# Kernel tuning notes

Hardware: AMD Instinct MI355X
Metric: run time of the kernel (lower is better)

The kernel has to match this reference:

```python
import jax, jax.numpy as jnp
import numpy as np

N = 50000      # nodes
E = 400000     # edges (before self-loops)
IN = 128       # in_channels
H = 4          # heads
C = 64         # hidden_channels == out_channels (per head)
ELI = 200000   # link-prediction query edges
NEG_SLOPE = 0.2
EPS = 1e-5


def setup_inputs():
    key = jax.random.key(0)
    ks = jax.random.split(key, 20)
    sc = 0.05
    inp = {}
    inp["x"] = jax.random.normal(ks[0], (N, IN), jnp.float32)
    inp["edge_index"] = jax.random.randint(ks[1], (2, E), 0, N)
    inp["edge_label_index"] = jax.random.randint(ks[2], (2, ELI), 0, N)
    # layer 1 GATv2 params
    inp["Wl1"] = jax.random.normal(ks[3], (IN, H * C), jnp.float32) * sc
    inp["bl1"] = jnp.zeros((H * C,), jnp.float32)
    inp["Wr1"] = jax.random.normal(ks[4], (IN, H * C), jnp.float32) * sc
    inp["br1"] = jnp.zeros((H * C,), jnp.float32)
    inp["att1"] = jax.random.normal(ks[5], (H, C), jnp.float32) * sc
    inp["bias1"] = jnp.zeros((C,), jnp.float32)
    # norm1 (BatchNorm affine)
    inp["g1"] = jnp.ones((C,), jnp.float32)
    inp["b1"] = jnp.zeros((C,), jnp.float32)
    # residual projection 1 (in_channels 128 -> hidden_dim 64)
    inp["Wres"] = jax.random.normal(ks[6], (IN, C), jnp.float32) * sc
    inp["bres"] = jnp.zeros((C,), jnp.float32)
    # layer 2 GATv2 params (hidden_dim 64 -> out 64)
    inp["Wl2"] = jax.random.normal(ks[7], (C, H * C), jnp.float32) * sc
    inp["bl2"] = jnp.zeros((H * C,), jnp.float32)
    inp["Wr2"] = jax.random.normal(ks[8], (C, H * C), jnp.float32) * sc
    inp["br2"] = jnp.zeros((H * C,), jnp.float32)
    inp["att2"] = jax.random.normal(ks[9], (H, C), jnp.float32) * sc
    inp["bias2"] = jnp.zeros((C,), jnp.float32)
    # norm2
    inp["g2"] = jnp.ones((C,), jnp.float32)
    inp["b2"] = jnp.zeros((C,), jnp.float32)
    return inp


def _gatv2(x, src, dst, Wl, bl, Wr, br, att, bias, n):
    # PyG GATv2Conv, concat=False (mean over heads), dropout off (eval)
    xl = (x @ Wl + bl).reshape(n, H, -1)   # source transform
    xr = (x @ Wr + br).reshape(n, H, -1)   # target transform
    e = jax.nn.leaky_relu(xl[src] + xr[dst], NEG_SLOPE)      # [E,H,C]
    logits = jnp.einsum('ehc,hc->eh', e, att)                # [E,H]
    m = jax.ops.segment_max(logits, dst, num_segments=n)     # segment softmax
    p = jnp.exp(logits - m[dst])
    s = jax.ops.segment_sum(p, dst, num_segments=n)
    alpha = p / s[dst]                                       # [E,H]
    out = jax.ops.segment_sum(xl[src] * alpha[:, :, None], dst, num_segments=n)
    return out.mean(axis=1) + bias                           # [N,C]


def _bn(x, g, b):
    mu = x.mean(axis=0)
    var = x.var(axis=0)
    return g * (x - mu) * jax.lax.rsqrt(var + EPS) + b


def reference(x, edge_index, edge_label_index,
              Wl1, bl1, Wr1, br1, att1, bias1, g1, b1, Wres, bres,
              Wl2, bl2, Wr2, br2, att2, bias2, g2, b2):
    loop = jnp.arange(N)
    src = jnp.concatenate([edge_index[0], loop])  # add_self_loops=True
    dst = jnp.concatenate([edge_index[1], loop])
    x_res = x @ Wres + bres
    h = _gatv2(x, src, dst, Wl1, bl1, Wr1, br1, att1, bias1, N)
    h = jax.nn.relu(_bn(h, g1, b1) + x_res)
    # res_proj2 is Identity (hidden_dim == out_dim)
    h2 = _gatv2(h, src, dst, Wl2, bl2, Wr2, br2, att2, bias2, N)
    z = _bn(h2, g2, b2) + h
    scores = (z[edge_label_index[0]] * z[edge_label_index[1]]).sum(axis=-1)
    return jax.nn.sigmoid(scores)
```

## Files before the change

### kernel.cpp

```cpp
#include <hip/hip_runtime.h>
#include <math.h>

#define NN 50000
#define EE 400000
#define ETOT 450000
#define INC 128
#define CC 64
#define HC 256
#define ELI_N 200000
#define MPAD 50176

typedef unsigned short u16;
typedef __attribute__((ext_vector_type(8))) short short8v;
typedef __attribute__((ext_vector_type(8))) unsigned short u16x8;
typedef __attribute__((ext_vector_type(4))) float f32x4;
typedef __attribute__((ext_vector_type(4))) unsigned short u16x4;

__device__ __forceinline__ u16 f2b(float v){
    unsigned u = __float_as_uint(v);
    u = (u + 0x7fffu + ((u >> 16) & 1u)) >> 16;
    return (u16)u;
}
__device__ __forceinline__ float b2f(u16 h){
    return __uint_as_float(((unsigned)h) << 16);
}
__device__ __forceinline__ u16 f2h(float v){
    _Float16 h = (_Float16)v; u16 r; __builtin_memcpy(&r, &h, 2); return r;
}
__device__ __forceinline__ float h2f(u16 h){
    _Float16 x; __builtin_memcpy(&x, &h, 2); return (float)x;
}
__device__ __forceinline__ f32x4 h2f4(u16x4 r){
    f32x4 o; o[0]=h2f(r[0]); o[1]=h2f(r[1]); o[2]=h2f(r[2]); o[3]=h2f(r[3]); return o;
}

__global__ void k_setup(const float* __restrict__ x, const int* __restrict__ ei,
                        const float* __restrict__ Wl1, const float* __restrict__ Wr1,
                        const float* __restrict__ Wres, const float* __restrict__ Wl2,
                        const float* __restrict__ Wr2,
                        u16* __restrict__ xhi, u16* __restrict__ xlo,
                        u16* __restrict__ hl1, u16* __restrict__ ll1,
                        u16* __restrict__ hr1, u16* __restrict__ lr1,
                        u16* __restrict__ hres, u16* __restrict__ lres,
                        u16* __restrict__ hl2, u16* __restrict__ ll2,
                        u16* __restrict__ hr2, u16* __restrict__ lr2,
                        int* __restrict__ deg){
    int gid = blockIdx.x*256 + threadIdx.x;
    if (gid < 800000){
        int row = gid >> 4;
        int k0  = (gid & 15) * 8;
        const float* ap = x + (size_t)row*128 + k0;
        float4 v0 = *(const float4*)ap;
        float4 v1 = *(const float4*)(ap + 4);
        float vv[8] = {v0.x, v0.y, v0.z, v0.w, v1.x, v1.y, v1.z, v1.w};
        u16x8 h8, l8;
        #pragma unroll
        for (int j = 0; j < 8; j++){
            u16 h = f2b(vv[j]);
            h8[j] = h;
            l8[j] = f2b(vv[j] - b2f(h));
        }
        size_t blk = (size_t)(row >> 4)*4 + (k0 >> 5);
        size_t addr = blk*512 + (size_t)((row & 15) + 16*((k0 >> 3) & 3))*8;
        *(u16x8*)(xhi + addr) = h8;
        *(u16x8*)(xlo + addr) = l8;
    } else if (gid < 906496){
        int g = gid - 800000;
        const float* src; u16* dh; u16* dl; int K, N, idx;
        if      (g <  32768){ src=Wl1;  dh=hl1;  dl=ll1;  K=128; N=256; idx=g; }
        else if (g <  65536){ src=Wr1;  dh=hr1;  dl=lr1;  K=128; N=256; idx=g-32768; }
        else if (g <  73728){ src=Wres; dh=hres; dl=lres; K=128; N=64;  idx=g-65536; }
        else if (g <  90112){ src=Wl2;  dh=hl2;  dl=ll2;  K=64;  N=256; idx=g-73728; }
        else                { src=Wr2;  dh=hr2;  dl=lr2;  K=64;  N=256; idx=g-90112; }
        int k = idx / N, n = idx - k*N;
        float v = src[idx];
        u16 h = f2b(v);
        size_t blk = (size_t)(n >> 4)*(K >> 5) + (k >> 5);
        size_t addr = blk*512 + (size_t)((n & 15) + 16*((k >> 3) & 3))*8 + (k & 7);
        dh[addr] = h;
        dl[addr] = f2b(v - b2f(h));
    } else if (gid < 1306496){
        int e = gid - 906496;
        atomicAdd(&deg[ei[EE + e]], 1);
    }
}

__global__ void k_scanA(const int* __restrict__ deg, int* __restrict__ iscan, int* __restrict__ part){
    __shared__ int sh[256];
    int tid = threadIdx.x;
    int base = blockIdx.x*1024 + tid*4;
    int v[4]; int t = 0;
    #pragma unroll
    for (int i = 0; i < 4; i++){ int idx = base + i; v[i] = (idx < NN) ? deg[idx]+1 : 0; t += v[i]; }
    sh[tid] = t; __syncthreads();
    for (int off = 1; off < 256; off <<= 1){
        int u = (tid >= off) ? sh[tid - off] : 0;
        __syncthreads();
        sh[tid] += u;
        __syncthreads();
    }
    int incl = sh[tid];
    int run = incl - t;
    #pragma unroll
    for (int i = 0; i < 4; i++){
        run += v[i];
        int idx = base + i;
        if (idx < NN) iscan[idx] = run;
    }
    if (tid == 255) part[blockIdx.x] = incl;
}

__global__ void k_scanC(const int* __restrict__ iscan, const int* __restrict__ part,
                        const int* __restrict__ deg, int* __restrict__ rowptr, int* __restrict__ cursor){
    int chunk = blockIdx.x >> 2;
    int ps = 0;
    for (int j = 0; j < chunk; j++) ps += part[j];
    int i = blockIdx.x*256 + threadIdx.x;
    if (i < NN){
        int v = iscan[i] + ps;
        rowptr[i+1] = v;
        cursor[i] = v - (deg[i]+1);
    }
    if (i == 0) rowptr[0] = 0;
}

__global__ void k_fill(const int* __restrict__ ei, int* __restrict__ cursor, int* __restrict__ csr_src){
    int idx = blockIdx.x*256 + threadIdx.x;
    if (idx >= ETOT) return;
    int s, d;
    if (idx < EE){ s = ei[idx]; d = ei[EE + idx]; }
    else         { s = idx - EE; d = s; }
    int pos = atomicAdd(&cursor[d], 1);
    csr_src[pos] = s;
}

#define LSTR 80

__global__ __launch_bounds__(256) void k_gemm1(const u16* __restrict__ Ahi, const u16* __restrict__ Alo,
        const u16* __restrict__ Whl1, const u16* __restrict__ Wll1,
        const u16* __restrict__ Whr1, const u16* __restrict__ Wlr1,
        const u16* __restrict__ Whres,const u16* __restrict__ Wlres,
        const float* __restrict__ bl1, const float* __restrict__ br1, const float* __restrict__ bres,
        u16* __restrict__ xl, u16* __restrict__ xr, u16* __restrict__ xres)
{
    __shared__ u16 stg[4][64*LSTR];
    int b = blockIdx.x;
    int c = b & 7;
    int k = b >> 3;
    int tile = k % 9;
    int sx = c + 8*(k/9);
    if (sx >= 196) return;
    int wid = threadIdx.x >> 6, lane = threadIdx.x & 63;
    const u16 *Bh, *Bl; const float* bias; u16* Cout; int n0, N;
    if (tile < 4)      { Bh=Whl1;  Bl=Wll1;  bias=bl1;  Cout=xl;   n0=tile*64;     N=256; }
    else if (tile < 8) { Bh=Whr1;  Bl=Wlr1;  bias=br1;  Cout=xr;   n0=(tile-4)*64; N=256; }
    else               { Bh=Whres; Bl=Wlres; bias=bres; Cout=xres; n0=0;           N=64;  }
    int rm0 = (sx*4 + wid) * 64;
    int rblk0 = rm0 >> 4;
    int nblk0 = n0 >> 4;
    int lr = lane & 15;
    f32x4 acc[4][4] = {};
    #pragma unroll
    for (int ks = 0; ks < 4; ks++){
        short8v ah[4], al[4], bh[4], blo[4];
        #pragma unroll
        for (int mf = 0; mf < 4; mf++){
            size_t addr = ((size_t)(rblk0 + mf)*4 + ks)*512 + (size_t)lane*8;
            ah[mf] = *(const short8v*)(Ahi + addr);
            al[mf] = *(const short8v*)(Alo + addr);
        }
        #pragma unroll
        for (int nf = 0; nf < 4; nf++){
            size_t addr = ((size_t)(nblk0 + nf)*4 + ks)*512 + (size_t)lane*8;
            bh[nf]  = *(const short8v*)(Bh + addr);
            blo[nf] = *(const short8v*)(Bl + addr);
        }
        #pragma unroll
        for (int mf = 0; mf < 4; mf++)
            #pragma unroll
            for (int nf = 0; nf < 4; nf++){
                acc[mf][nf] = __builtin_amdgcn_mfma_f32_16x16x32_bf16(ah[mf], bh[nf],  acc[mf][nf], 0, 0, 0);
                acc[mf][nf] = __builtin_amdgcn_mfma_f32_16x16x32_bf16(al[mf], bh[nf],  acc[mf][nf], 0, 0, 0);
                acc[mf][nf] = __builtin_amdgcn_mfma_f32_16x16x32_bf16(ah[mf], blo[nf], acc[mf][nf], 0, 0, 0);
            }
    }
    int rbase = (lane >> 4) << 2;
    u16* my = &stg[wid][0];
    #pragma unroll
    for (int nf = 0; nf < 4; nf++){
        int col = nf*16 + lr;
        float bv = bias[n0 + col];
        #pragma unroll
        for (int mf = 0; mf < 4; mf++){
            #pragma unroll
            for (int r = 0; r < 4; r++){
                int row = mf*16 + rbase + r;
                my[row*LSTR + col] = f2h(acc[mf][nf][r] + bv);
            }
        }
    }
    __syncthreads();
    int rl = lane >> 3, cl = lane & 7;
    #pragma unroll
    for (int it = 0; it < 8; it++){
        int row = it*8 + rl;
        u16x8 v = *(u16x8*)&my[row*LSTR + cl*8];
        int grow = rm0 + row;
        if (grow < NN) *(u16x8*)(Cout + (size_t)grow*N + n0 + cl*8) = v;
    }
}

__global__ __launch_bounds__(256) void k_gemm2(const u16* __restrict__ Ahi, const u16* __restrict__ Alo,
        const u16* __restrict__ Whl2, const u16* __restrict__ Wll2,
        const u16* __restrict__ Whr2, const u16* __restrict__ Wlr2,
        const float* __restrict__ bl2, const float* __restrict__ br2,
        u16* __restrict__ xl, u16* __restrict__ xr)
{
    __shared__ u16 stg[4][64*LSTR];
    int b = blockIdx.x;
    int c = b & 7;
    int k = b >> 3;
    int tile = k & 7;
    int sx = c + 8*(k >> 3);
    if (sx >= 196) return;
    int wid = threadIdx.x >> 6, lane = threadIdx.x & 63;
    const u16 *Bh, *Bl; const float* bias; u16* Cout;
    if (tile < 4){ Bh=Whl2; Bl=Wll2; bias=bl2; Cout=xl; }
    else         { Bh=Whr2; Bl=Wlr2; bias=br2; Cout=xr; }
    int n0 = (tile & 3)*64;
    int rm0 = (sx*4 + wid) * 64;
    int rblk0 = rm0 >> 4;
    int nblk0 = n0 >> 4;
    int lr = lane & 15;
    f32x4 acc[4][4] = {};
    #pragma unroll
    for (int ks = 0; ks < 2; ks++){
        short8v ah[4], al[4], bh[4], blo[4];
        #pragma unroll
        for (int mf = 0; mf < 4; mf++){
            size_t addr = ((size_t)(rblk0 + mf)*2 + ks)*512 + (size_t)lane*8;
            ah[mf] = *(const short8v*)(Ahi + addr);
            al[mf] = *(const short8v*)(Alo + addr);
        }
        #pragma unroll
        for (int nf = 0; nf < 4; nf++){
            size_t addr = ((size_t)(nblk0 + nf)*2 + ks)*512 + (size_t)lane*8;
            bh[nf]  = *(const short8v*)(Bh + addr);
            blo[nf] = *(const short8v*)(Bl + addr);
        }
        #pragma unroll
        for (int mf = 0; mf < 4; mf++)
            #pragma unroll
            for (int nf = 0; nf < 4; nf++){
                acc[mf][nf] = __builtin_amdgcn_mfma_f32_16x16x32_bf16(ah[mf], bh[nf],  acc[mf][nf], 0, 0, 0);
                acc[mf][nf] = __builtin_amdgcn_mfma_f32_16x16x32_bf16(al[mf], bh[nf],  acc[mf][nf], 0, 0, 0);
                acc[mf][nf] = __builtin_amdgcn_mfma_f32_16x16x32_bf16(ah[mf], blo[nf], acc[mf][nf], 0, 0, 0);
            }
    }
    int rbase = (lane >> 4) << 2;
    u16* my = &stg[wid][0];
    #pragma unroll
    for (int nf = 0; nf < 4; nf++){
        int col = nf*16 + lr;
        float bv = bias[n0 + col];
        #pragma unroll
        for (int mf = 0; mf < 4; mf++){
            #pragma unroll
            for (int r = 0; r < 4; r++){
                int row = mf*16 + rbase + r;
                my[row*LSTR + col] = f2h(acc[mf][nf][r] + bv);
            }
        }
    }
    __syncthreads();
    int rl = lane >> 3, cl = lane & 7;
    #pragma unroll
    for (int it = 0; it < 8; it++){
        int row = it*8 + rl;
        u16x8 v = *(u16x8*)&my[row*LSTR + cl*8];
        int grow = rm0 + row;
        if (grow < NN) *(u16x8*)(Cout + (size_t)grow*256 + n0 + cl*8) = v;
    }
}

__global__ __launch_bounds__(256) void k_gat(const u16* __restrict__ xl, const u16* __restrict__ xr,
                                             const int* __restrict__ csr_src, const int* __restrict__ rowptr,
                                             const float* __restrict__ att, const float* __restrict__ bias,
                                             float* __restrict__ out,
                                             float* __restrict__ part_s, float* __restrict__ part_q)
{
    __shared__ float ls[4][64];
    __shared__ float lq[4][64];
    int wave = threadIdx.x >> 6, lane = threadIdx.x & 63;
    int node = blockIdx.x*4 + wave;
    int p0 = rowptr[node], p1 = rowptr[node+1];
    f32x4 xrf  = h2f4(*(const u16x4*)(xr + (size_t)node*HC + 4*lane));
    f32x4 attf = *(const f32x4*)(att + 4*lane);
    float s = 0.f;
    f32x4 acc = {0.f, 0.f, 0.f, 0.f};
    int p = p0;
    for (; p + 4 <= p1; p += 4){
        int i0 = csr_src[p], i1 = csr_src[p+1], i2 = csr_src[p+2], i3 = csr_src[p+3];
        f32x4 x0 = h2f4(*(const u16x4*)(xl + (size_t)i0*HC + 4*lane));
        f32x4 x1 = h2f4(*(const u16x4*)(xl + (size_t)i1*HC + 4*lane));
        f32x4 x2 = h2f4(*(const u16x4*)(xl + (size_t)i2*HC + 4*lane));
        f32x4 x3 = h2f4(*(const u16x4*)(xl + (size_t)i3*HC + 4*lane));
        float t0 = 0.f, t1 = 0.f, t2 = 0.f, t3 = 0.f;
        #pragma unroll
        for (int j = 0; j < 4; j++){
            float e0 = x0[j] + xrf[j]; e0 = (e0 > 0.f) ? e0 : 0.2f*e0; t0 += e0*attf[j];
            float e1 = x1[j] + xrf[j]; e1 = (e1 > 0.f) ? e1 : 0.2f*e1; t1 += e1*attf[j];
            float e2 = x2[j] + xrf[j]; e2 = (e2 > 0.f) ? e2 : 0.2f*e2; t2 += e2*attf[j];
            float e3 = x3[j] + xrf[j]; e3 = (e3 > 0.f) ? e3 : 0.2f*e3; t3 += e3*attf[j];
        }
        #pragma unroll
        for (int off = 1; off < 16; off <<= 1){
            t0 += __shfl_xor(t0, off, 64);
            t1 += __shfl_xor(t1, off, 64);
            t2 += __shfl_xor(t2, off, 64);
            t3 += __shfl_xor(t3, off, 64);
        }
        float w0 = __expf(t0), w1 = __expf(t1), w2 = __expf(t2), w3 = __expf(t3);
        s += (w0 + w1) + (w2 + w3);
        acc = acc + x0*w0 + x1*w1 + x2*w2 + x3*w3;
    }
    for (; p < p1; p++){
        int i0 = csr_src[p];
        f32x4 x0 = h2f4(*(const u16x4*)(xl + (size_t)i0*HC + 4*lane));
        float t0 = 0.f;
        #pragma unroll
        for (int j = 0; j < 4; j++){ float e0 = x0[j] + xrf[j]; e0 = (e0 > 0.f) ? e0 : 0.2f*e0; t0 += e0*attf[j]; }
        #pragma unroll
        for (int off = 1; off < 16; off <<= 1) t0 += __shfl_xor(t0, off, 64);
        float w0 = __expf(t0);
        s += w0;
        acc = acc + x0*w0;
    }
    float inv = 1.f / s;
    f32x4 o = acc * inv;
    #pragma unroll
    for (int j = 0; j < 4; j++){ o[j] += __shfl_xor(o[j], 16, 64); o[j] += __shfl_xor(o[j], 32, 64); }
    if (lane < 16){
        f32x4 bv = *(const f32x4*)(bias + 4*lane);
        f32x4 res = o*0.25f + bv;
        *(f32x4*)(out + (size_t)node*CC + 4*lane) = res;
        #pragma unroll
        for (int j = 0; j < 4; j++){
            ls[wave][4*lane + j] = res[j];
            lq[wave][4*lane + j] = res[j]*res[j];
        }
    }
    __syncthreads();
    int tid = threadIdx.x;
    if (tid < 128){
        int c = tid & 63;
        if (tid < 64){
            float v = (ls[0][c] + ls[1][c]) + (ls[2][c] + ls[3][c]);
            atomicAdd(&part_s[(blockIdx.x & 63)*64 + c], v);
        } else {
            float v = (lq[0][c] + lq[1][c]) + (lq[2][c] + lq[3][c]);
            atomicAdd(&part_q[(blockIdx.x & 63)*64 + c], v);
        }
    }
}

__global__ __launch_bounds__(256) void k_post1(const float* __restrict__ hraw, const u16* __restrict__ xres,
                        const float* __restrict__ part_s, const float* __restrict__ part_q,
                        const float* __restrict__ g, const float* __restrict__ b,
                        u16* __restrict__ h16, u16* __restrict__ hhi, u16* __restrict__ hlo){
    __shared__ float red[128];
    int tid = threadIdx.x;
    if (tid < 128){
        const float* base = (tid < 64) ? part_s : part_q;
        int c = tid & 63;
        float sv = 0.f;
        for (int bb = 0; bb < 64; bb++) sv += base[bb*64 + c];
        red[tid] = sv;
    }
    __syncthreads();
    int i = blockIdx.x*256 + tid;
    if (i >= NN*16) return;
    float4 hv = ((const float4*)hraw)[i];
    f32x4 rp = h2f4(*(const u16x4*)(xres + (size_t)i*4));
    int row = i >> 4;
    int c0 = (i & 15) * 4;
    float hp[4] = {hv.x, hv.y, hv.z, hv.w};
    u16x4 h4, l4, hh4;
    const float invN = 1.f / (float)NN;
    #pragma unroll
    for (int k = 0; k < 4; k++){
        int c = c0 + k;
        float mean = red[c] * invN;
        float var  = red[64 + c] * invN - mean*mean;
        float rstd = rsqrtf(var + 1e-5f);
        float v = g[c]*(hp[k] - mean)*rstd + b[c] + rp[k];
        v = (v > 0.f) ? v : 0.f;
        hh4[k] = f2h(v);
        u16 h = f2b(v);
        h4[k] = h;
        l4[k] = f2b(v - b2f(h));
    }
    *(u16x4*)(h16 + (size_t)i*4) = hh4;
    size_t blk = (size_t)(row >> 4)*2 + (c0 >> 5);
    size_t addr = blk*512 + (size_t)((row & 15) + 16*((c0 >> 3) & 3))*8 + (c0 & 7);
    *(u16x4*)(hhi + addr) = h4;
    *(u16x4*)(hlo + addr) = l4;
}

__global__ __launch_bounds__(256) void k_post2(const float* __restrict__ hraw, const u16* __restrict__ h16,
                        const float* __restrict__ part_s, const float* __restrict__ part_q,
                        const float* __restrict__ g, const float* __restrict__ b,
                        u16* __restrict__ zout){
    __shared__ float red[128];
    int tid = threadIdx.x;
    if (tid < 128){
        const float* base = (tid < 64) ? part_s : part_q;
        int c = tid & 63;
        float sv = 0.f;
        for (int bb = 0; bb < 64; bb++) sv += base[bb*64 + c];
        red[tid] = sv;
    }
    __syncthreads();
    int i = blockIdx.x*256 + tid;
    if (i >= NN*16) return;
    float4 hv = ((const float4*)hraw)[i];
    f32x4 rp = h2f4(*(const u16x4*)(h16 + (size_t)i*4));
    int c0 = (i & 15) * 4;
    float hp[4] = {hv.x, hv.y, hv.z, hv.w};
    u16x4 res;
    const float invN = 1.f / (float)NN;
    #pragma unroll
    for (int k = 0; k < 4; k++){
        int c = c0 + k;
        float mean = red[c] * invN;
        float var  = red[64 + c] * invN - mean*mean;
        float rstd = rsqrtf(var + 1e-5f);
        res[k] = f2h(g[c]*(hp[k] - mean)*rstd + b[c] + rp[k]);
    }
    *(u16x4*)(zout + (size_t)i*4) = res;
}

__global__ __launch_bounds__(256) void k_score(const u16* __restrict__ z, const int* __restrict__ eli,
                                               float* __restrict__ out){
    int t = blockIdx.x*256 + threadIdx.x;
    int i = t >> 4; int j = t & 15;
    if (i >= ELI_N) return;
    int a = eli[i], b = eli[ELI_N + i];
    f32x4 va = h2f4(*(const u16x4*)(z + (size_t)a*64 + j*4));
    f32x4 vb = h2f4(*(const u16x4*)(z + (size_t)b*64 + j*4));
    float s = va[0]*vb[0] + va[1]*vb[1] + va[2]*vb[2] + va[3]*vb[3];
    #pragma unroll
    for (int off = 8; off > 0; off >>= 1) s += __shfl_xor(s, off, 64);
    if (j == 0) out[i] = 1.f / (1.f + __expf(-s));
}

extern "C" void kernel_launch(void* const* d_in, const int* in_sizes, int n_in,
                              void* d_out, int out_size, void* d_ws, size_t ws_size,
                              hipStream_t stream) {
    const float* x    = (const float*)d_in[0];
    const int*   ei   = (const int*)  d_in[1];
    const int*   eli  = (const int*)  d_in[2];
    const float* Wl1  = (const float*)d_in[3];
    const float* bl1  = (const float*)d_in[4];
    const float* Wr1  = (const float*)d_in[5];
    const float* br1  = (const float*)d_in[6];
    const float* att1 = (const float*)d_in[7];
    const float* bias1= (const float*)d_in[8];
    const float* g1   = (const float*)d_in[9];
    const float* b1   = (const float*)d_in[10];
    const float* Wres = (const float*)d_in[11];
    const float* bres = (const float*)d_in[12];
    const float* Wl2  = (const float*)d_in[13];
    const float* bl2  = (const float*)d_in[14];
    const float* Wr2  = (const float*)d_in[15];
    const float* br2  = (const float*)d_in[16];
    const float* att2 = (const float*)d_in[17];
    const float* bias2= (const float*)d_in[18];
    const float* g2   = (const float*)d_in[19];
    const float* b2   = (const float*)d_in[20];
    float* out = (float*)d_out;

    char* w = (char*)d_ws;
    size_t o = 0;
    auto take = [&](size_t bytes)->char*{ char* p = w + o; o += (bytes + 255) & ~(size_t)255; return p; };
    u16*  xl   = (u16*) take((size_t)NN*HC*2);
    u16*  xr   = (u16*) take((size_t)NN*HC*2);
    u16*  xres = (u16*) take((size_t)NN*CC*2);
    float* hraw = (float*)take((size_t)NN*CC*4);
    u16*  h16  = (u16*) take((size_t)NN*CC*2);
    u16*  z16  = (u16*) take((size_t)NN*CC*2);
    u16*  xhi  = (u16*)take((size_t)MPAD*INC*2);
    u16*  xlo  = (u16*)take((size_t)MPAD*INC*2);
    u16*  hhi  = (u16*)take((size_t)MPAD*CC*2);
    u16*  hlo  = (u16*)take((size_t)MPAD*CC*2);
    u16* whl1 = (u16*)take(256*128*2);  u16* wll1 = (u16*)take(256*128*2);
    u16* whr1 = (u16*)take(256*128*2);  u16* wlr1 = (u16*)take(256*128*2);
    u16* whres= (u16*)take(64*128*2);   u16* wlres= (u16*)take(64*128*2);
    u16* whl2 = (u16*)take(256*64*2);   u16* wll2 = (u16*)take(256*64*2);
    u16* whr2 = (u16*)take(256*64*2);   u16* wlr2 = (u16*)take(256*64*2);
    char* zreg  = take(4*64*64*4 + (size_t)NN*4);
    float* ps1  = (float*)zreg;
    float* pq1  = ps1 + 4096;
    float* ps2  = ps1 + 8192;
    float* pq2  = ps1 + 12288;
    int* deg    = (int*)(zreg + 4*64*64*4);
    int* rowptr = (int*)take((size_t)(NN+1)*4);
    int* iscan  = (int*)take((size_t)NN*4);
    int* cursor = (int*)take((size_t)NN*4);
    int* csr_src= (int*)take((size_t)ETOT*4);
    int* part   = (int*)take(64*4);

    hipMemsetAsync(zreg, 0, 4*64*64*4 + (size_t)NN*4, stream);

    k_setup<<<5104, 256, 0, stream>>>(x, ei, Wl1, Wr1, Wres, Wl2, Wr2,
                                      xhi, xlo,
                                      whl1, wll1, whr1, wlr1, whres, wlres,
                                      whl2, wll2, whr2, wlr2, deg);

    k_scanA<<<49, 256, 0, stream>>>(deg, iscan, part);
    k_scanC<<<196, 256, 0, stream>>>(iscan, part, deg, rowptr, cursor);
    k_fill<<<(ETOT+255)/256, 256, 0, stream>>>(ei, cursor, csr_src);

    k_gemm1<<<1800, 256, 0, stream>>>(xhi, xlo, whl1, wll1, whr1, wlr1, whres, wlres,
                                      bl1, br1, bres, xl, xr, xres);
    k_gat<<<NN/4, 256, 0, stream>>>(xl, xr, csr_src, rowptr, att1, bias1, hraw, ps1, pq1);
    k_post1<<<(NN*16+255)/256, 256, 0, stream>>>(hraw, xres, ps1, pq1, g1, b1, h16, hhi, hlo);

    k_gemm2<<<1600, 256, 0, stream>>>(hhi, hlo, whl2, wll2, whr2, wlr2, bl2, br2, xl, xr);
    k_gat<<<NN/4, 256, 0, stream>>>(xl, xr, csr_src, rowptr, att2, bias2, hraw, ps2, pq2);
    k_post2<<<(NN*16+255)/256, 256, 0, stream>>>(hraw, h16, ps2, pq2, g2, b2, z16);

    k_score<<<(ELI_N*16+255)/256, 256, 0, stream>>>(z16, eli, out);
}
```

Baseline: 248.5 us.

## Split GAT wave into two half-waves processing two edges each with fp16 dot2

Restructures the GAT aggregation kernel so each wave is split into two 32-lane halves, each handling a different edge with 8 channels per lane (16-byte loads). The attention logit is computed in packed fp16 with fdot2 and a shorter shuffle reduction, and the two halves' partial sums are combined at the end. This aims to increase memory-level parallelism per gather and cut the ALU and shuffle work per edge. In exchange, the leaky-relu and dot product now run in fp16, which lowers precision, and the tail loop masks out-of-range edges.

Result: faster. 233.4 us, median of 2 (-6.1%).

```diff
diff --git a/kernel.cpp b/kernel.cpp
--- a/kernel.cpp
+++ b/kernel.cpp
@@ -14,7 +14,11 @@
 typedef __attribute__((ext_vector_type(8))) short short8v;
 typedef __attribute__((ext_vector_type(8))) unsigned short u16x8;
 typedef __attribute__((ext_vector_type(4))) float f32x4;
+typedef __attribute__((ext_vector_type(8))) float f32x8;
 typedef __attribute__((ext_vector_type(4))) unsigned short u16x4;
+typedef __attribute__((ext_vector_type(4))) _Float16 h16x4;
+typedef __attribute__((ext_vector_type(2))) _Float16 h16x2;
+typedef __attribute__((ext_vector_type(8))) _Float16 h16x8;
 
 __device__ __forceinline__ u16 f2b(float v){
     unsigned u = __float_as_uint(v);
@@ -294,60 +298,80 @@
     int wave = threadIdx.x >> 6, lane = threadIdx.x & 63;
     int node = blockIdx.x*4 + wave;
     int p0 = rowptr[node], p1 = rowptr[node+1];
-    f32x4 xrf  = h2f4(*(const u16x4*)(xr + (size_t)node*HC + 4*lane));
-    f32x4 attf = *(const f32x4*)(att + 4*lane);
+    int sub = lane >> 5;
+    int q   = lane & 31;
+    h16x8 xrh = *(const h16x8*)(xr + (size_t)node*HC + 8*q);
+    f32x4 a0 = *(const f32x4*)(att + 8*q);
+    f32x4 a1 = *(const f32x4*)(att + 8*q + 4);
+    h16x2 aa0, aa1, aa2, aa3;
+    aa0[0]=(_Float16)a0[0]; aa0[1]=(_Float16)a0[1];
+    aa1[0]=(_Float16)a0[2]; aa1[1]=(_Float16)a0[3];
+    aa2[0]=(_Float16)a1[0]; aa2[1]=(_Float16)a1[1];
+    aa3[0]=(_Float16)a1[2]; aa3[1]=(_Float16)a1[3];
     float s = 0.f;
-    f32x4 acc = {0.f, 0.f, 0.f, 0.f};
+    f32x8 acc = {0.f,0.f,0.f,0.f,0.f,0.f,0.f,0.f};
     int p = p0;
     for (; p + 4 <= p1; p += 4){
-        int i0 = csr_src[p], i1 = csr_src[p+1], i2 = csr_src[p+2], i3 = csr_src[p+3];
-        f32x4 x0 = h2f4(*(const u16x4*)(xl + (size_t)i0*HC + 4*lane));
-        f32x4 x1 = h2f4(*(const u16x4*)(xl + (size_t)i1*HC + 4*lane));
-        f32x4 x2 = h2f4(*(const u16x4*)(xl + (size_t)i2*HC + 4*lane));
-        f32x4 x3 = h2f4(*(const u16x4*)(xl + (size_t)i3*HC + 4*lane));
-        float t0 = 0.f, t1 = 0.f, t2 = 0.f, t3 = 0.f;
-        #pragma unroll
-        for (int j = 0; j < 4; j++){
-            float e0 = x0[j] + xrf[j]; e0 = (e0 > 0.f) ? e0 : 0.2f*e0; t0 += e0*attf[j];
-            float e1 = x1[j] + xrf[j]; e1 = (e1 > 0.f) ? e1 : 0.2f*e1; t1 += e1*attf[j];
-            float e2 = x2[j] + xrf[j]; e2 = (e2 > 0.f) ? e2 : 0.2f*e2; t2 += e2*attf[j];
-            float e3 = x3[j] + xrf[j]; e3 = (e3 > 0.f) ? e3 : 0.2f*e3; t3 += e3*attf[j];
-        }
-        #pragma unroll
-        for (int off = 1; off < 16; off <<= 1){
-            t0 += __shfl_xor(t0, off, 64);
-            t1 += __shfl_xor(t1, off, 64);
-            t2 += __shfl_xor(t2, off, 64);
-            t3 += __shfl_xor(t3, off, 64);
-        }
-        float w0 = __expf(t0), w1 = __expf(t1), w2 = __expf(t2), w3 = __expf(t3);
-        s += (w0 + w1) + (w2 + w3);
-        acc = acc + x0*w0 + x1*w1 + x2*w2 + x3*w3;
-    }
-    for (; p < p1; p++){
-        int i0 = csr_src[p];
-        f32x4 x0 = h2f4(*(const u16x4*)(xl + (size_t)i0*HC + 4*lane));
-        float t0 = 0.f;
-        #pragma unroll
-        for (int j = 0; j < 4; j++){ float e0 = x0[j] + xrf[j]; e0 = (e0 > 0.f) ? e0 : 0.2f*e0; t0 += e0*attf[j]; }
-        #pragma unroll
-        for (int off = 1; off < 16; off <<= 1) t0 += __shfl_xor(t0, off, 64);
-        float w0 = __expf(t0);
-        s += w0;
-        acc = acc + x0*w0;
-    }
+        int ia = csr_src[p + sub];
+        int ib = csr_src[p + 2 + sub];
+        h16x8 xa = *(const h16x8*)(xl + (size_t)ia*HC + 8*q);
+        h16x8 xb = *(const h16x8*)(xl + (size_t)ib*HC + 8*q);
+        h16x8 ea = xa + xrh, eb = xb + xrh;
+        h16x8 la = __builtin_elementwise_max(ea, ea * (_Float16)0.2f);
+        h16x8 lb = __builtin_elementwise_max(eb, eb * (_Float16)0.2f);
+        float ta = __builtin_amdgcn_fdot2(__builtin_shufflevector(la,la,0,1), aa0, 0.f, false);
+        float tb = __builtin_amdgcn_fdot2(__builtin_shufflevector(lb,lb,0,1), aa0, 0.f, false);
+        ta = __builtin_amdgcn_fdot2(__builtin_shufflevector(la,la,2,3), aa1, ta, false);
+        tb = __builtin_amdgcn_fdot2(__builtin_shufflevector(lb,lb,2,3), aa1, tb, false);
+        ta = __builtin_amdgcn_fdot2(__builtin_shufflevector(la,la,4,5), aa2, ta, false);
+        tb = __builtin_amdgcn_fdot2(__builtin_shufflevector(lb,lb,4,5), aa2, tb, false);
+        ta = __builtin_amdgcn_fdot2(__builtin_shufflevector(la,la,6,7), aa3, ta, false);
+        tb = __builtin_amdgcn_fdot2(__builtin_shufflevector(lb,lb,6,7), aa3, tb, false);
+        #pragma unroll
+        for (int off = 1; off < 8; off <<= 1){
+            ta += __shfl_xor(ta, off, 64);
+            tb += __shfl_xor(tb, off, 64);
+        }
+        float wa = __expf(ta), wb = __expf(tb);
+        s += wa + wb;
+        f32x8 fa = __builtin_convertvector(xa, f32x8);
+        f32x8 fb = __builtin_convertvector(xb, f32x8);
+        acc = acc + fa*wa + fb*wb;
+    }
+    for (; p < p1; p += 2){
+        int idx = p + sub;
+        bool ok = idx < p1;
+        int ia = csr_src[ok ? idx : p];
+        h16x8 xa = *(const h16x8*)(xl + (size_t)ia*HC + 8*q);
+        h16x8 ea = xa + xrh;
+        h16x8 la = __builtin_elementwise_max(ea, ea * (_Float16)0.2f);
+        float ta = __builtin_amdgcn_fdot2(__builtin_shufflevector(la,la,0,1), aa0, 0.f, false);
+        ta = __builtin_amdgcn_fdot2(__builtin_shufflevector(la,la,2,3), aa1, ta, false);
+        ta = __builtin_amdgcn_fdot2(__builtin_shufflevector(la,la,4,5), aa2, ta, false);
+        ta = __builtin_amdgcn_fdot2(__builtin_shufflevector(la,la,6,7), aa3, ta, false);
+        #pragma unroll
+        for (int off = 1; off < 8; off <<= 1) ta += __shfl_xor(ta, off, 64);
+        float wa = ok ? __expf(ta) : 0.f;
+        s += wa;
+        acc = acc + __builtin_convertvector(xa, f32x8)*wa;
+    }
+    s += __shfl_xor(s, 32, 64);
+    #pragma unroll
+    for (int j = 0; j < 8; j++) acc[j] += __shfl_xor(acc[j], 32, 64);
     float inv = 1.f / s;
-    f32x4 o = acc * inv;
-    #pragma unroll
-    for (int j = 0; j < 4; j++){ o[j] += __shfl_xor(o[j], 16, 64); o[j] += __shfl_xor(o[j], 32, 64); }
-    if (lane < 16){
-        f32x4 bv = *(const f32x4*)(bias + 4*lane);
-        f32x4 res = o*0.25f + bv;
-        *(f32x4*)(out + (size_t)node*CC + 4*lane) = res;
-        #pragma unroll
-        for (int j = 0; j < 4; j++){
-            ls[wave][4*lane + j] = res[j];
-            lq[wave][4*lane + j] = res[j]*res[j];
+    f32x8 o = acc * inv;
+    #pragma unroll
+    for (int j = 0; j < 8; j++){ o[j] += __shfl_xor(o[j], 8, 64); o[j] += __shfl_xor(o[j], 16, 64); }
+    if (lane < 8){
+        float bb[8];
+        #pragma unroll
+        for (int j = 0; j < 8; j++) bb[j] = o[j]*0.25f + bias[8*lane + j];
+        *(float4*)(out + (size_t)node*CC + 8*lane)     = make_float4(bb[0],bb[1],bb[2],bb[3]);
+        *(float4*)(out + (size_t)node*CC + 8*lane + 4) = make_float4(bb[4],bb[5],bb[6],bb[7]);
+        #pragma unroll
+        for (int j = 0; j < 8; j++){
+            ls[wave][8*lane + j] = bb[j];
+            lq[wave][8*lane + j] = bb[j]*bb[j];
         }
     }
     __syncthreads();
```
